# Kernel optimization log

Measured on AMD Instinct MI355X. Metric: run time of the kernel, lower is better.

## Reference

```python
import jax, jax.numpy as jnp
import numpy as np

V = 10000
E = 60000
B = 8
LATENT = 512
HIDDEN = 256
NUM_LAYERS = 5


def setup_inputs() -> dict:
    key = jax.random.key(0)
    ks = jax.random.split(key, 12)
    vertex_xyz = jax.random.normal(ks[0], (V, 3), dtype=jnp.float32)
    latent = jax.random.normal(ks[1], (B, LATENT), dtype=jnp.float32)
    edge_index = jax.random.randint(ks[2], (2, E), 0, V, dtype=jnp.int64)
    s = 0.02
    input_W = jax.random.normal(ks[3], (HIDDEN, LATENT + 3), dtype=jnp.float32) * s
    input_b = jnp.zeros((HIDDEN,), dtype=jnp.float32)
    conv_W = jax.random.normal(ks[4], (NUM_LAYERS, HIDDEN, HIDDEN), dtype=jnp.float32) * s
    conv_b = jnp.zeros((NUM_LAYERS, HIDDEN), dtype=jnp.float32)
    out_W = jax.random.normal(ks[5], (3, HIDDEN), dtype=jnp.float32) * s
    out_b = jnp.zeros((3,), dtype=jnp.float32)
    return dict(vertex_xyz=vertex_xyz, latent=latent, edge_index=edge_index,
                input_W=input_W, input_b=input_b, conv_W=conv_W, conv_b=conv_b,
                out_W=out_W, out_b=out_b)


def _gcn_norm(edge_index, num_nodes):
    # PyG GCNConv default: add self-loops, symmetric normalization.
    src, dst = edge_index[0], edge_index[1]
    loop = jnp.arange(num_nodes, dtype=src.dtype)
    src = jnp.concatenate([src, loop])
    dst = jnp.concatenate([dst, loop])
    deg = jax.ops.segment_sum(jnp.ones_like(dst, dtype=jnp.float32), dst,
                              num_segments=num_nodes)
    dinv = jnp.where(deg > 0, jax.lax.rsqrt(deg), 0.0)
    norm = dinv[src] * dinv[dst]  # [E+V]
    return src, dst, norm


def reference(vertex_xyz, latent, edge_index, input_W, input_b, conv_W, conv_b, out_W, out_b):
    Bn, Vn = latent.shape[0], vertex_xyz.shape[0]
    # Build node features: concat template xyz with broadcast latent -> [B, V, 3+latent]
    x = jnp.concatenate([
        jnp.broadcast_to(vertex_xyz[None], (Bn, Vn, 3)),
        jnp.broadcast_to(latent[:, None, :], (Bn, Vn, latent.shape[1])),
    ], axis=-1)
    x = jax.nn.relu(jnp.einsum('bvf,hf->bvh', x, input_W) + input_b)

    # The batched edge_index is a per-graph copy offset by b*V, so normalization
    # and message passing are identical per batch; vectorize over B.
    src, dst, norm = _gcn_norm(edge_index, Vn)
    for l in range(conv_W.shape[0]):
        h = jnp.einsum('bvh,oh->bvo', x, conv_W[l])        # linear transform
        msg = h[:, src, :] * norm[None, :, None]           # gather + scale
        agg = jnp.zeros_like(h).at[:, dst, :].add(msg)     # scatter-add
        x = jax.nn.relu(agg + conv_b[l])

    disp = jnp.einsum('bvh,oh->bvo', x, out_W) + out_b     # [B, V, 3]
    return disp
```

## Files before the change

kernel.cpp:

```cpp
#include <hip/hip_runtime.h>

#define Vn 10000
#define En 60000
#define Bb 8
#define LAT 512
#define HID 256
#define NL 5
#define Mrows (Bb * Vn)

typedef __attribute__((ext_vector_type(4))) int    i32x4;
typedef __attribute__((ext_vector_type(4))) float  f32x4;
typedef __attribute__((ext_vector_type(8))) short  bf16x8;
typedef __attribute__((ext_vector_type(4))) unsigned short u16x4;

__device__ __forceinline__ float bf2f(unsigned short u) {
    union { unsigned int u; float f; } c;
    c.u = ((unsigned int)u) << 16;
    return c.f;
}
__device__ __forceinline__ unsigned short f2bf(float f) {
    union { float f; unsigned int u; } c;
    c.f = f;
    unsigned int u = c.u + 0x7FFFu + ((c.u >> 16) & 1u);
    return (unsigned short)(u >> 16);
}


__global__ void k_init(int* cnt, int* cur) {
    int i = blockIdx.x * blockDim.x + threadIdx.x;
    if (i < Vn) { cnt[i] = 0; cur[i] = 0; }
}

__global__ void k_count(const int* __restrict__ dst, int* __restrict__ cnt) {
    int e = blockIdx.x * blockDim.x + threadIdx.x;
    if (e < En) atomicAdd(&cnt[dst[e]], 1);
}

__global__ void k_scan(const int* __restrict__ cnt, int* __restrict__ rowptr,
                       float* __restrict__ dinv, float* __restrict__ selfn) {
    __shared__ int part[1024];
    const int PER = 10;
    int tid = threadIdx.x;
    int base = tid * PER;
    int local[PER];
    int s = 0;
#pragma unroll
    for (int i = 0; i < PER; ++i) {
        int idx = base + i;
        int c = (idx < Vn) ? cnt[idx] : 0;
        if (idx < Vn) {
            float d = (float)c + 1.0f;
            float r = rsqrtf(d);
            dinv[idx] = r;
            selfn[idx] = r * r;
        }
        local[i] = s;
        s += c;
    }
    part[tid] = s;
    __syncthreads();
    for (int off = 1; off < 1024; off <<= 1) {
        int add = (tid >= off) ? part[tid - off] : 0;
        __syncthreads();
        part[tid] += add;
        __syncthreads();
    }
    int chunk_base = part[tid] - s;
#pragma unroll
    for (int i = 0; i < PER; ++i) {
        int idx = base + i;
        if (idx < Vn) rowptr[idx] = chunk_base + local[i];
    }
    if (tid == 1023) rowptr[Vn] = part[1023];
}

__global__ void k_fill(const int* __restrict__ src, const int* __restrict__ dst,
                       const float* __restrict__ dinv, const int* __restrict__ rowptr,
                       int* __restrict__ cur, int* __restrict__ csr_src,
                       float* __restrict__ csr_norm) {
    int e = blockIdx.x * blockDim.x + threadIdx.x;
    if (e < En) {
        int s = src[e], d = dst[e];
        int p = atomicAdd(&cur[d], 1);
        int idx = rowptr[d] + p;
        csr_src[idx] = s;
        csr_norm[idx] = dinv[s] * dinv[d];
    }
}


__global__ __launch_bounds__(256) void k_prep(const float* __restrict__ conv_W,
                                              unsigned short* __restrict__ Wb,
                                              const float* __restrict__ latent,
                                              const float* __restrict__ input_W,
                                              const float* __restrict__ input_b,
                                              float* __restrict__ latc,
                                              float* __restrict__ w3p) {
    int blk = blockIdx.x;
    if (blk < 1280) {
        int i = blk * 256 + threadIdx.x;
        Wb[i] = f2bf(conv_W[i]);
        return;
    }
    int gid = (blk - 1280) * 256 + threadIdx.x;
    int q = gid & 3;
    int i = gid >> 2;
    int b = i >> 8, h = i & 255;
    const float* wr = input_W + (size_t)h * (LAT + 3) + 3 + q * 128;
    const float* lr = latent + (size_t)b * LAT + q * 128;
    float s = 0.0f;
#pragma unroll 8
    for (int k = 0; k < 128; ++k) s = fmaf(lr[k], wr[k], s);
    s += __shfl_xor(s, 1, 64);
    s += __shfl_xor(s, 2, 64);
    if (q == 0) latc[i] = s + input_b[h];
    if (gid < 768) w3p[gid] = input_W[(size_t)(gid & 255) * (LAT + 3) + (gid >> 8)];
}

__global__ __launch_bounds__(256) void k_input(const float* __restrict__ xyz,
                                               const float* __restrict__ w3p,
                                               const float* __restrict__ latc,
                                               unsigned short* __restrict__ X) {
    int gid = blockIdx.x * 256 + threadIdx.x;
    int row = gid >> 5;
    int hc = (gid & 31) << 3;
    int b = row / Vn;
    int v = row - b * Vn;
    float x0 = xyz[v * 3 + 0], x1 = xyz[v * 3 + 1], x2 = xyz[v * 3 + 2];
    const float* lc = latc + b * HID + hc;
    u16x4 o0, o1;
#pragma unroll
    for (int j = 0; j < 8; ++j) {
        float s = lc[j];
        s = fmaf(x0, w3p[hc + j], s);
        s = fmaf(x1, w3p[256 + hc + j], s);
        s = fmaf(x2, w3p[512 + hc + j], s);
        unsigned short r = f2bf(fmaxf(s, 0.0f));
        if (j < 4) o0[j] = r; else o1[j - 4] = r;
    }
    u16x4* dst = (u16x4*)&X[(size_t)row * HID + hc];
    dst[0] = o0;
    dst[1] = o1;
}


__global__ __launch_bounds__(256) void k_agg(const unsigned short* __restrict__ Xin,
                                             unsigned short* __restrict__ Xa,
                                             const int* __restrict__ rowptr,
                                             const int* __restrict__ csr_src,
                                             const float* __restrict__ csr_norm,
                                             const float* __restrict__ selfn) {
    int wid = threadIdx.x >> 6;
    int lane = threadIdx.x & 63;
    int bv = blockIdx.x * 4 + wid;
    int b = bv / Vn;
    int v = bv - b * Vn;
    int f = lane << 2;
    size_t bbase = (size_t)b * Vn * HID;

    u16x4 hs = *(const u16x4*)&Xin[(size_t)bv * HID + f];
    float sn = selfn[v];
    float a0 = sn * bf2f(hs[0]), a1 = sn * bf2f(hs[1]);
    float a2 = sn * bf2f(hs[2]), a3 = sn * bf2f(hs[3]);

    int s = rowptr[v], e = rowptr[v + 1];
    int i = s;
    for (; i + 2 <= e; i += 2) {
        float n0 = csr_norm[i], n1 = csr_norm[i + 1];
        int s0 = csr_src[i], s1 = csr_src[i + 1];
        u16x4 h0 = *(const u16x4*)&Xin[bbase + (size_t)s0 * HID + f];
        u16x4 h1 = *(const u16x4*)&Xin[bbase + (size_t)s1 * HID + f];
        a0 = fmaf(n0, bf2f(h0[0]), a0); a1 = fmaf(n0, bf2f(h0[1]), a1);
        a2 = fmaf(n0, bf2f(h0[2]), a2); a3 = fmaf(n0, bf2f(h0[3]), a3);
        a0 = fmaf(n1, bf2f(h1[0]), a0); a1 = fmaf(n1, bf2f(h1[1]), a1);
        a2 = fmaf(n1, bf2f(h1[2]), a2); a3 = fmaf(n1, bf2f(h1[3]), a3);
    }
    if (i < e) {
        float n0 = csr_norm[i];
        u16x4 h0 = *(const u16x4*)&Xin[bbase + (size_t)csr_src[i] * HID + f];
        a0 = fmaf(n0, bf2f(h0[0]), a0); a1 = fmaf(n0, bf2f(h0[1]), a1);
        a2 = fmaf(n0, bf2f(h0[2]), a2); a3 = fmaf(n0, bf2f(h0[3]), a3);
    }
    u16x4 r;
    r[0] = f2bf(a0); r[1] = f2bf(a1); r[2] = f2bf(a2); r[3] = f2bf(a3);
    *(u16x4*)&Xa[(size_t)bv * HID + f] = r;
}


__global__ __launch_bounds__(256) void k_gemm(const unsigned short* __restrict__ A,
                                              const unsigned short* __restrict__ Wb,
                                              const float* __restrict__ bias,
                                              unsigned short* __restrict__ Xout) {
    __shared__ __align__(16) char smem[32768];
    const int t = threadIdx.x;
    const int w = t >> 6;
    const int l = t & 63;
    const int m0 = blockIdx.x * 64;
    const int n0w = w * 64;
    const int lr = l & 15;
    const int lg = l >> 4;

    i32x4 av[8];
    {
        const char* srcb = (const char*)(A + (size_t)m0 * HID);
#pragma unroll
        for (int i = 0; i < 8; ++i)
            av[i] = *(const i32x4*)(srcb + i * 4096 + t * 16);
    }

    bf16x8 Bf[4][8];
#pragma unroll
    for (int nt = 0; nt < 4; ++nt) {
        const unsigned short* wp = Wb + (size_t)(n0w + nt * 16 + lr) * HID + lg * 8;
#pragma unroll
        for (int ks = 0; ks < 8; ++ks)
            Bf[nt][ks] = __builtin_bit_cast(bf16x8, *(const i32x4*)(wp + ks * 32));
    }

#pragma unroll
    for (int i = 0; i < 8; ++i) {
        int x = i * 4096 + t * 16;
        int sw = (x & ~511) | ((x & 511) ^ (((x >> 9) & 15) << 4));
        *(i32x4*)(smem + sw) = av[i];
    }
    __syncthreads();

    f32x4 acc[4][4];
#pragma unroll
    for (int mt = 0; mt < 4; ++mt)
#pragma unroll
        for (int nt = 0; nt < 4; ++nt)
            acc[mt][nt] = (f32x4){0.f, 0.f, 0.f, 0.f};

#pragma unroll
    for (int ks = 0; ks < 8; ++ks) {
#pragma unroll
        for (int mt = 0; mt < 4; ++mt) {
            int row = mt * 16 + lr;
            int colb = ks * 64 + lg * 16;
            int addr = row * 512 + (colb ^ ((row & 15) << 4));
            bf16x8 a = __builtin_bit_cast(bf16x8, *(const i32x4*)(smem + addr));
#pragma unroll
            for (int nt = 0; nt < 4; ++nt)
                acc[mt][nt] = __builtin_amdgcn_mfma_f32_16x16x32_bf16(
                    Bf[nt][ks], a, acc[mt][nt], 0, 0, 0);
        }
    }

    __syncthreads();

    f32x4 bb[4];
#pragma unroll
    for (int nt = 0; nt < 4; ++nt)
        bb[nt] = *(const f32x4*)&bias[n0w + nt * 16 + lg * 4];

#pragma unroll
    for (int mt = 0; mt < 4; ++mt) {
        int row = mt * 16 + lr;
        int rs = (row & 15) << 4;
#pragma unroll
        for (int nt = 0; nt < 4; ++nt) {
            u16x4 ov;
#pragma unroll
            for (int r = 0; r < 4; ++r)
                ov[r] = f2bf(fmaxf(acc[mt][nt][r] + bb[nt][r], 0.0f));
            int colbyte = n0w * 2 + nt * 32 + lg * 8;
            int addr = row * 512 + (colbyte ^ rs);
            *(u16x4*)(smem + addr) = ov;
        }
    }
    __syncthreads();

    char* dstb = (char*)(Xout + (size_t)m0 * HID);
#pragma unroll
    for (int i = 0; i < 8; ++i) {
        int x = i * 4096 + t * 16;
        int sw = (x & ~511) | ((x & 511) ^ (((x >> 9) & 15) << 4));
        *(i32x4*)(dstb + x) = *(const i32x4*)(smem + sw);
    }
}


__global__ __launch_bounds__(256) void k_out(const unsigned short* __restrict__ X,
                                             const float* __restrict__ oW,
                                             const float* __restrict__ ob,
                                             float* __restrict__ disp) {
    int wid = threadIdx.x >> 6;
    int lane = threadIdx.x & 63;
    int bv = blockIdx.x * 4 + wid;
    int f = lane << 2;
    u16x4 xv = *(const u16x4*)&X[(size_t)bv * HID + f];
    float x0 = bf2f(xv[0]), x1 = bf2f(xv[1]), x2 = bf2f(xv[2]), x3 = bf2f(xv[3]);
    float p[3];
#pragma unroll
    for (int c = 0; c < 3; ++c) {
        f32x4 wv = *(const f32x4*)&oW[c * HID + f];
        p[c] = x0 * wv[0] + x1 * wv[1] + x2 * wv[2] + x3 * wv[3];
    }
#pragma unroll
    for (int off = 32; off > 0; off >>= 1) {
#pragma unroll
        for (int c = 0; c < 3; ++c) p[c] += __shfl_down(p[c], off, 64);
    }
    if (lane == 0) {
#pragma unroll
        for (int c = 0; c < 3; ++c) disp[(size_t)bv * 3 + c] = p[c] + ob[c];
    }
}


extern "C" void kernel_launch(void* const* d_in, const int* in_sizes, int n_in,
                              void* d_out, int out_size, void* d_ws, size_t ws_size,
                              hipStream_t stream) {
    const float* xyz     = (const float*)d_in[0];
    const float* latent  = (const float*)d_in[1];
    const int*   eidx    = (const int*)d_in[2];
    const float* input_W = (const float*)d_in[3];
    const float* input_b = (const float*)d_in[4];
    const float* conv_W  = (const float*)d_in[5];
    const float* conv_b  = (const float*)d_in[6];
    const float* out_W   = (const float*)d_in[7];
    const float* out_b   = (const float*)d_in[8];
    float* disp = (float*)d_out;

    const int* src = eidx;
    const int* dst = eidx + En;

    char* base = (char*)d_ws;
    size_t off = 0;
    auto alloc = [&](size_t bytes) {
        size_t o = off;
        off = (off + bytes + 255) & ~(size_t)255;
        return (void*)(base + o);
    };
    int*   cnt      = (int*)alloc(Vn * 4);
    int*   cur      = (int*)alloc(Vn * 4);
    float* dinv     = (float*)alloc(Vn * 4);
    float* selfn    = (float*)alloc(Vn * 4);
    int*   rowptr   = (int*)alloc((Vn + 1) * 4);
    int*   csr_src  = (int*)alloc(En * 4);
    float* csr_norm = (float*)alloc(En * 4);
    float* latc     = (float*)alloc(Bb * HID * 4);
    float* w3p      = (float*)alloc(3 * HID * 4);
    unsigned short* Wb = (unsigned short*)alloc((size_t)NL * HID * HID * 2);
    unsigned short* X  = (unsigned short*)alloc((size_t)Mrows * HID * 2);
    unsigned short* Xa = (unsigned short*)alloc((size_t)Mrows * HID * 2);

    k_init<<<(Vn + 255) / 256, 256, 0, stream>>>(cnt, cur);
    k_count<<<(En + 255) / 256, 256, 0, stream>>>(dst, cnt);
    k_scan<<<1, 1024, 0, stream>>>(cnt, rowptr, dinv, selfn);
    k_fill<<<(En + 255) / 256, 256, 0, stream>>>(src, dst, dinv, rowptr, cur, csr_src, csr_norm);

    k_prep<<<1312, 256, 0, stream>>>(conv_W, Wb, latent, input_W, input_b, latc, w3p);

    k_input<<<Mrows * 32 / 256, 256, 0, stream>>>(xyz, w3p, latc, X);

    for (int l = 0; l < NL; ++l) {
        k_agg<<<Mrows / 4, 256, 0, stream>>>(X, Xa, rowptr, csr_src, csr_norm, selfn);
        k_gemm<<<Mrows / 64, 256, 0, stream>>>(Xa, Wb + (size_t)l * HID * HID,
                                               conv_b + (size_t)l * HID, X);
    }

    k_out<<<Mrows / 4, 256, 0, stream>>>(X, out_W, out_b, disp);
}
```

Before: 516.6 us.

## Interleave batch dimension into node rows so aggregation reads contiguous per-vertex blocks

Changes the activation layout from [B][V][H] to [V][B][H], so all 8 batch copies of a vertex sit in one contiguous 4KB block. The aggregation kernel now runs one wave per vertex and handles all batches at once: each CSR edge's index and norm are loaded once, and four 16-byte vector loads per lane fetch the whole neighbour block. This removes the repeated CSR traversal across batches and makes the gather reads contiguous and wide. The cost is 32 accumulators per lane, which raises register pressure, and fewer waves in the aggregation grid. The input and output kernels are updated to the new row mapping; the GEMM is unaffected because it is row-independent.

```diff
diff --git a/kernel.cpp b/kernel.cpp
--- a/kernel.cpp
+++ b/kernel.cpp
@@ -8,10 +8,12 @@
 #define NL 5
 #define Mrows (Bb * Vn)
 
+
 typedef __attribute__((ext_vector_type(4))) int    i32x4;
 typedef __attribute__((ext_vector_type(4))) float  f32x4;
 typedef __attribute__((ext_vector_type(8))) short  bf16x8;
 typedef __attribute__((ext_vector_type(4))) unsigned short u16x4;
+typedef __attribute__((ext_vector_type(8))) unsigned short u16x8;
 
 __device__ __forceinline__ float bf2f(unsigned short u) {
     union { unsigned int u; float f; } c;
@@ -124,8 +126,8 @@
     int gid = blockIdx.x * 256 + threadIdx.x;
     int row = gid >> 5;
     int hc = (gid & 31) << 3;
-    int b = row / Vn;
-    int v = row - b * Vn;
+    int v = row >> 3;
+    int b = row & 7;
     float x0 = xyz[v * 3 + 0], x1 = xyz[v * 3 + 1], x2 = xyz[v * 3 + 2];
     const float* lc = latc + b * HID + hc;
     u16x4 o0, o1;
@@ -152,38 +154,44 @@
                                              const float* __restrict__ selfn) {
     int wid = threadIdx.x >> 6;
     int lane = threadIdx.x & 63;
-    int bv = blockIdx.x * 4 + wid;
-    int b = bv / Vn;
-    int v = bv - b * Vn;
-    int f = lane << 2;
-    size_t bbase = (size_t)b * Vn * HID;
-
-    u16x4 hs = *(const u16x4*)&Xin[(size_t)bv * HID + f];
+    int v = blockIdx.x * 4 + wid;
+
+    float acc[4][8];
+    const u16x8* sp = (const u16x8*)(Xin + (size_t)v * (8 * HID));
     float sn = selfn[v];
-    float a0 = sn * bf2f(hs[0]), a1 = sn * bf2f(hs[1]);
-    float a2 = sn * bf2f(hs[2]), a3 = sn * bf2f(hs[3]);
+#pragma unroll
+    for (int c = 0; c < 4; ++c) {
+        u16x8 hv = sp[c * 64 + lane];
+#pragma unroll
+        for (int j = 0; j < 8; ++j) acc[c][j] = sn * bf2f(hv[j]);
+    }
 
     int s = rowptr[v], e = rowptr[v + 1];
-    int i = s;
-    for (; i + 2 <= e; i += 2) {
-        float n0 = csr_norm[i], n1 = csr_norm[i + 1];
-        int s0 = csr_src[i], s1 = csr_src[i + 1];
-        u16x4 h0 = *(const u16x4*)&Xin[bbase + (size_t)s0 * HID + f];
-        u16x4 h1 = *(const u16x4*)&Xin[bbase + (size_t)s1 * HID + f];
-        a0 = fmaf(n0, bf2f(h0[0]), a0); a1 = fmaf(n0, bf2f(h0[1]), a1);
-        a2 = fmaf(n0, bf2f(h0[2]), a2); a3 = fmaf(n0, bf2f(h0[3]), a3);
-        a0 = fmaf(n1, bf2f(h1[0]), a0); a1 = fmaf(n1, bf2f(h1[1]), a1);
-        a2 = fmaf(n1, bf2f(h1[2]), a2); a3 = fmaf(n1, bf2f(h1[3]), a3);
-    }
-    if (i < e) {
-        float n0 = csr_norm[i];
-        u16x4 h0 = *(const u16x4*)&Xin[bbase + (size_t)csr_src[i] * HID + f];
-        a0 = fmaf(n0, bf2f(h0[0]), a0); a1 = fmaf(n0, bf2f(h0[1]), a1);
-        a2 = fmaf(n0, bf2f(h0[2]), a2); a3 = fmaf(n0, bf2f(h0[3]), a3);
-    }
-    u16x4 r;
-    r[0] = f2bf(a0); r[1] = f2bf(a1); r[2] = f2bf(a2); r[3] = f2bf(a3);
-    *(u16x4*)&Xa[(size_t)bv * HID + f] = r;
+    for (int i = s; i < e; ++i) {
+        float nm = csr_norm[i];
+        const u16x8* up = (const u16x8*)(Xin + (size_t)csr_src[i] * (8 * HID));
+        u16x8 h0 = up[0 * 64 + lane];
+        u16x8 h1 = up[1 * 64 + lane];
+        u16x8 h2 = up[2 * 64 + lane];
+        u16x8 h3 = up[3 * 64 + lane];
+#pragma unroll
+        for (int j = 0; j < 8; ++j) acc[0][j] = fmaf(nm, bf2f(h0[j]), acc[0][j]);
+#pragma unroll
+        for (int j = 0; j < 8; ++j) acc[1][j] = fmaf(nm, bf2f(h1[j]), acc[1][j]);
+#pragma unroll
+        for (int j = 0; j < 8; ++j) acc[2][j] = fmaf(nm, bf2f(h2[j]), acc[2][j]);
+#pragma unroll
+        for (int j = 0; j < 8; ++j) acc[3][j] = fmaf(nm, bf2f(h3[j]), acc[3][j]);
+    }
+
+    u16x8* op = (u16x8*)(Xa + (size_t)v * (8 * HID));
+#pragma unroll
+    for (int c = 0; c < 4; ++c) {
+        u16x8 ov;
+#pragma unroll
+        for (int j = 0; j < 8; ++j) ov[j] = f2bf(acc[c][j]);
+        op[c * 64 + lane] = ov;
+    }
 }
 
 
@@ -287,9 +295,11 @@
                                              float* __restrict__ disp) {
     int wid = threadIdx.x >> 6;
     int lane = threadIdx.x & 63;
-    int bv = blockIdx.x * 4 + wid;
+    int row = blockIdx.x * 4 + wid;
+    int v = row >> 3;
+    int b = row & 7;
     int f = lane << 2;
-    u16x4 xv = *(const u16x4*)&X[(size_t)bv * HID + f];
+    u16x4 xv = *(const u16x4*)&X[(size_t)row * HID + f];
     float x0 = bf2f(xv[0]), x1 = bf2f(xv[1]), x2 = bf2f(xv[2]), x3 = bf2f(xv[3]);
     float p[3];
 #pragma unroll
@@ -304,7 +314,8 @@
     }
     if (lane == 0) {
 #pragma unroll
-        for (int c = 0; c < 3; ++c) disp[(size_t)bv * 3 + c] = p[c] + ob[c];
+        for (int c = 0; c < 3; ++c)
+            disp[((size_t)b * Vn + v) * 3 + c] = p[c] + ob[c];
     }
 }
 
@@ -356,7 +367,7 @@
     k_input<<<Mrows * 32 / 256, 256, 0, stream>>>(xyz, w3p, latc, X);
 
     for (int l = 0; l < NL; ++l) {
-        k_agg<<<Mrows / 4, 256, 0, stream>>>(X, Xa, rowptr, csr_src, csr_norm, selfn);
+        k_agg<<<Vn / 4, 256, 0, stream>>>(X, Xa, rowptr, csr_src, csr_norm, selfn);
         k_gemm<<<Mrows / 64, 256, 0, stream>>>(Xa, Wb + (size_t)l * HID * HID,
                                                conv_b + (size_t)l * HID, X);
     }
```

Measured after the change: 527.7 us. +2.2%, slower.
